# Kernel optimization log

Measured on AMD Instinct MI355X. Metric: run time of the kernel, lower is better.

## Reference

```python
import jax, jax.numpy as jnp
import numpy as np

N_NODES = 50000
N_EDGES = 640000
WIDTH = 128
K = 5
N_CONVS = 6  # 1 input + 4 hidden + 1 output ChebConv layers


def setup_inputs() -> dict:
    key = jax.random.key(0)
    k1, k2, k3, k4 = jax.random.split(key, 4)
    scale = 1.0 / np.sqrt(WIDTH)
    x = jax.random.normal(k1, (N_NODES, WIDTH), dtype=jnp.float32)
    edge_index = jax.random.randint(k2, (2, N_EDGES), 0, N_NODES, dtype=jnp.int64)
    conv_w = jax.random.normal(k3, (N_CONVS, K, WIDTH, WIDTH), dtype=jnp.float32) * scale
    conv_b = jnp.zeros((N_CONVS, WIDTH), dtype=jnp.float32)
    lin_w = jax.random.normal(k4, (WIDTH, 1), dtype=jnp.float32) * scale
    lin_b = jnp.zeros((1,), dtype=jnp.float32)
    return {"x": x, "edge_index": edge_index, "conv_w": conv_w,
            "conv_b": conv_b, "lin_w": lin_w, "lin_b": lin_b}


def _cheb_norm(edge_index):
    # PyG ChebConv with normalization='sym', lambda_max=2.0:
    # L_hat = 2/lambda_max * (I - D^-1/2 A D^-1/2) - I = -D^-1/2 A D^-1/2
    # (diagonal terms cancel), so per-edge weight = -d_i^-1/2 * d_j^-1/2.
    src, dst = edge_index[0], edge_index[1]
    ones = jnp.ones((edge_index.shape[1],), dtype=jnp.float32)
    deg = jax.ops.segment_sum(ones, dst, num_segments=N_NODES)
    d_inv_sqrt = jnp.where(deg > 0, jax.lax.rsqrt(jnp.maximum(deg, 1e-12)), 0.0)
    return -d_inv_sqrt[src] * d_inv_sqrt[dst]


def _propagate(x, src, dst, norm):
    # L_hat @ x via gather -> weight -> scatter-add
    msg = norm[:, None] * x[src]              # [E, C]
    return jax.ops.segment_sum(msg, dst, num_segments=N_NODES)


def _cheb_conv(x, W, b, src, dst, norm):
    # Chebyshev recurrence: T0=x, T1=Lx, Tk = 2*L*T(k-1) - T(k-2)
    Tx0 = x
    out = Tx0 @ W[0]
    Tx1 = _propagate(Tx0, src, dst, norm)
    out = out + Tx1 @ W[1]
    for k in range(2, K):
        Tx2 = 2.0 * _propagate(Tx1, src, dst, norm) - Tx0
        out = out + Tx2 @ W[k]
        Tx0, Tx1 = Tx1, Tx2
    return out + b


def reference(x, edge_index, conv_w, conv_b, lin_w, lin_b):
    src, dst = edge_index[0], edge_index[1]
    norm = _cheb_norm(edge_index)
    h = x
    # first 5 convs followed by ReLU (dropout is identity in eval mode)
    for l in range(N_CONVS - 1):
        h = _cheb_conv(h, conv_w[l], conv_b[l], src, dst, norm)
        h = jax.nn.relu(h)
    # final conv (no activation) + Linear(128, 1)
    h = _cheb_conv(h, conv_w[N_CONVS - 1], conv_b[N_CONVS - 1], src, dst, norm)
    return h @ lin_w + lin_b
```

## Files before the change

### kernel.cpp

```cpp
#include <hip/hip_runtime.h>


#define NN 50000
#define NE 640000
#define WID 128
#define PROP_BLOCKS 2048

typedef __attribute__((ext_vector_type(8))) short bf16x8;
typedef __attribute__((ext_vector_type(4))) float f32x4;

__device__ __forceinline__ unsigned short f2bf(float f) {
  union { float f; unsigned int u; } v; v.f = f;
  unsigned int r = v.u + 0x7FFF + ((v.u >> 16) & 1);
  return (unsigned short)(r >> 16);
}
__device__ __forceinline__ unsigned int pack2(float lo, float hi) {
  return (unsigned int)f2bf(lo) | ((unsigned int)f2bf(hi) << 16);
}
__device__ __forceinline__ float bflo(unsigned int u) {
  return __uint_as_float(u << 16);
}
__device__ __forceinline__ float bfhi(unsigned int u) {
  return __uint_as_float(u & 0xffff0000u);
}
__device__ __forceinline__ float dec_norm(unsigned int p) {
  unsigned int lo = p & 0xfffu;
  float v = -__uint_as_float(((112u + ((p >> 8) & 15u)) << 23) | ((p & 255u) << 15));
  return (lo == 0u) ? 0.f : v;
}


__global__ __launch_bounds__(256) void degree_kernel(const int* __restrict__ ei,
                                                     int* __restrict__ deg, int E) {
  int e = blockIdx.x * 256 + threadIdx.x;
  if (e < E) atomicAdd(&deg[ei[E + e]], 1);
}

__global__ __launch_bounds__(256) void scan1_kernel(const int* __restrict__ deg,
                                                    int* __restrict__ lex,
                                                    int* __restrict__ bsum,
                                                    float* __restrict__ dinv, int n) {
  __shared__ int ws[4];
  int tid = threadIdx.x, lane = tid & 63, w = tid >> 6;
  int i = blockIdx.x * 256 + tid;
  int cnt = (i < n) ? deg[i] : 0;
  if (i < n) {
    float d = (float)cnt;
    dinv[i] = d > 0.0f ? rsqrtf(d) : 0.0f;
  }
  int v = cnt;
#pragma unroll
  for (int off = 1; off < 64; off <<= 1) {
    int u = __shfl_up(v, off, 64);
    if (lane >= off) v += u;
  }
  if (lane == 63) ws[w] = v;
  __syncthreads();
  int wexcl = 0;
#pragma unroll
  for (int k = 0; k < 4; ++k) wexcl += (k < w) ? ws[k] : 0;
  if (i < n) lex[i] = wexcl + v - cnt;
  if (tid == 255) bsum[blockIdx.x] = wexcl + v;
}

__global__ __launch_bounds__(256) void scan2_kernel(const int* __restrict__ bsum,
                                                    int* __restrict__ boff,
                                                    int* __restrict__ row_end, int nb) {
  __shared__ int ws[4];
  int tid = threadIdx.x, lane = tid & 63, w = tid >> 6;
  int cnt = (tid < nb) ? bsum[tid] : 0;
  int v = cnt;
#pragma unroll
  for (int off = 1; off < 64; off <<= 1) {
    int u = __shfl_up(v, off, 64);
    if (lane >= off) v += u;
  }
  if (lane == 63) ws[w] = v;
  __syncthreads();
  int wexcl = 0;
#pragma unroll
  for (int k = 0; k < 4; ++k) wexcl += (k < w) ? ws[k] : 0;
  if (tid < nb) boff[tid] = wexcl + v - cnt;
  if (tid == 255) *row_end = wexcl + v;
}

__global__ __launch_bounds__(256) void scan3_kernel(const int* __restrict__ lex,
                                                    const int* __restrict__ boff,
                                                    int* __restrict__ row_start,
                                                    int* __restrict__ fill_ptr, int n) {
  int i = blockIdx.x * 256 + threadIdx.x;
  if (i < n) {
    int rs = lex[i] + boff[blockIdx.x];
    row_start[i] = rs;
    fill_ptr[i] = rs;
  }
}

__global__ __launch_bounds__(256) void fill_kernel(const int* __restrict__ ei,
                                                   const float* __restrict__ dinv,
                                                   int* __restrict__ fill_ptr,
                                                   unsigned int* __restrict__ csr, int E) {
  int e = blockIdx.x * 256 + threadIdx.x;
  if (e < E) {
    int s = ei[e];
    int d = ei[E + e];
    int pos = atomicAdd(&fill_ptr[d], 1);
    float mag = dinv[s] * dinv[d];
    unsigned int bits = __float_as_uint(mag);
    unsigned int pk = (unsigned int)s << 12;
    if (bits != 0u) {
      bits += 0x4000u;
      int ex = (int)((bits >> 23) & 255u) - 112;
      ex = max(0, min(15, ex));
      pk |= ((unsigned int)ex << 8) | ((bits >> 15) & 0xffu);
    }
    csr[pos] = pk;
  }
}

__global__ __launch_bounds__(256) void cvt_kernel(const float* __restrict__ x,
                                                  unsigned short* __restrict__ xo,
                                                  const float* __restrict__ w,
                                                  unsigned short* __restrict__ wt,
                                                  int nx, int nw) {
  int i = blockIdx.x * 256 + threadIdx.x;
  if (i < nx) {
    xo[i] = f2bf(x[i]);
  } else if (i < nx + nw) {
    int j = i - nx;
    int l = j / (WID * 640);
    int r = j % (WID * 640);
    int col = r / 640;
    int k = r % 640;
    int kk = k >> 7, m = k & 127;
    wt[j] = f2bf(w[(((size_t)l * 5 + kk) * WID + m) * WID + col]);
  }
}


__global__ __launch_bounds__(256) void prop_kernel(unsigned short* __restrict__ out,
                                                   const unsigned short* __restrict__ xin,
                                                   const unsigned short* __restrict__ sub,
                                                   float scale,
                                                   const int* __restrict__ row_start,
                                                   const unsigned int* __restrict__ csr,
                                                   int n) {
  int t = threadIdx.x & 15;
  for (int node = blockIdx.x * 16 + (threadIdx.x >> 4); node < n;
       node += PROP_BLOCKS * 16) {
    int s = row_start[node], e = row_start[node + 1];
    float a0 = 0.f, a1 = 0.f, a2 = 0.f, a3 = 0.f;
    float a4 = 0.f, a5 = 0.f, a6 = 0.f, a7 = 0.f;
    for (int base = s; base < e; base += 16) {
      int cnt = min(16, e - base);
      unsigned int ed = (t < cnt) ? csr[base + t] : 0u;
      int j = 0;
      for (; j + 4 <= cnt; j += 4) {
        unsigned int p0 = (unsigned int)__shfl((int)ed, j, 16);
        unsigned int p1 = (unsigned int)__shfl((int)ed, j + 1, 16);
        unsigned int p2 = (unsigned int)__shfl((int)ed, j + 2, 16);
        unsigned int p3 = (unsigned int)__shfl((int)ed, j + 3, 16);
        int s0 = p0 >> 12, s1 = p1 >> 12, s2 = p2 >> 12, s3 = p3 >> 12;
        float n0 = dec_norm(p0), n1 = dec_norm(p1), n2 = dec_norm(p2), n3 = dec_norm(p3);
        const uint4 v0 = *(const uint4*)(xin + (size_t)s0 * WID + t * 8);
        const uint4 v1 = *(const uint4*)(xin + (size_t)s1 * WID + t * 8);
        const uint4 v2 = *(const uint4*)(xin + (size_t)s2 * WID + t * 8);
        const uint4 v3 = *(const uint4*)(xin + (size_t)s3 * WID + t * 8);
        a0 += n0 * bflo(v0.x) + n1 * bflo(v1.x) + n2 * bflo(v2.x) + n3 * bflo(v3.x);
        a1 += n0 * bfhi(v0.x) + n1 * bfhi(v1.x) + n2 * bfhi(v2.x) + n3 * bfhi(v3.x);
        a2 += n0 * bflo(v0.y) + n1 * bflo(v1.y) + n2 * bflo(v2.y) + n3 * bflo(v3.y);
        a3 += n0 * bfhi(v0.y) + n1 * bfhi(v1.y) + n2 * bfhi(v2.y) + n3 * bfhi(v3.y);
        a4 += n0 * bflo(v0.z) + n1 * bflo(v1.z) + n2 * bflo(v2.z) + n3 * bflo(v3.z);
        a5 += n0 * bfhi(v0.z) + n1 * bfhi(v1.z) + n2 * bfhi(v2.z) + n3 * bfhi(v3.z);
        a6 += n0 * bflo(v0.w) + n1 * bflo(v1.w) + n2 * bflo(v2.w) + n3 * bflo(v3.w);
        a7 += n0 * bfhi(v0.w) + n1 * bfhi(v1.w) + n2 * bfhi(v2.w) + n3 * bfhi(v3.w);
      }
      for (; j < cnt; ++j) {
        unsigned int pj = (unsigned int)__shfl((int)ed, j, 16);
        int sj = pj >> 12;
        float nj = dec_norm(pj);
        const uint4 v = *(const uint4*)(xin + (size_t)sj * WID + t * 8);
        a0 += nj * bflo(v.x); a1 += nj * bfhi(v.x);
        a2 += nj * bflo(v.y); a3 += nj * bfhi(v.y);
        a4 += nj * bflo(v.z); a5 += nj * bfhi(v.z);
        a6 += nj * bflo(v.w); a7 += nj * bfhi(v.w);
      }
    }
    size_t o = (size_t)node * WID + t * 8;
    float r0 = scale * a0, r1 = scale * a1, r2 = scale * a2, r3 = scale * a3;
    float r4 = scale * a4, r5 = scale * a5, r6 = scale * a6, r7 = scale * a7;
    if (sub) {
      const uint4 sv = *(const uint4*)(sub + o);
      r0 -= bflo(sv.x); r1 -= bfhi(sv.x);
      r2 -= bflo(sv.y); r3 -= bfhi(sv.y);
      r4 -= bflo(sv.z); r5 -= bfhi(sv.z);
      r6 -= bflo(sv.w); r7 -= bfhi(sv.w);
    }
    uint4 wv;
    wv.x = pack2(r0, r1); wv.y = pack2(r2, r3);
    wv.z = pack2(r4, r5); wv.w = pack2(r6, r7);
    *(uint4*)(out + o) = wv;
  }
}


__global__ __launch_bounds__(256) void cheb_gemm(
    const unsigned short* __restrict__ T0, const unsigned short* __restrict__ T1,
    const unsigned short* __restrict__ T2, const unsigned short* __restrict__ T3,
    const unsigned short* __restrict__ T4,
    const unsigned short* __restrict__ Wt,
    const float* __restrict__ bias,
    unsigned short* __restrict__ Hb,
    const float* __restrict__ linw, const float* __restrict__ linb,
    float* __restrict__ y, int M, int mode) {
  __shared__ unsigned short As[64][72];
  __shared__ unsigned short Bs[128][72];
  const unsigned short* chunks[5] = {T0, T1, T2, T3, T4};
  int tid = threadIdx.x;
  int wave = tid >> 6, lane = tid & 63;
  int lrow = lane & 15, quad = lane >> 4;
  int rowBase = blockIdx.x * 64;

  f32x4 acc[8];
#pragma unroll
  for (int b = 0; b < 8; ++b) acc[b] = (f32x4){0.f, 0.f, 0.f, 0.f};

  int ar = tid >> 2, aseg = (tid & 3) * 16;
  int agrow = min(rowBase + ar, M - 1);
  int bc = tid >> 1, bseg = (tid & 1) * 32;

  int4 aR0, aR1, bR0, bR1, bR2, bR3;
  {
    const unsigned short* ap = chunks[0] + (size_t)agrow * WID + aseg;
    aR0 = *(const int4*)ap;
    aR1 = *(const int4*)(ap + 8);
    const unsigned short* bp = Wt + (size_t)bc * 640 + bseg;
    bR0 = *(const int4*)bp;
    bR1 = *(const int4*)(bp + 8);
    bR2 = *(const int4*)(bp + 16);
    bR3 = *(const int4*)(bp + 24);
  }

  for (int kc = 0; kc < 10; ++kc) {
    *(int4*)(&As[ar][aseg]) = aR0;
    *(int4*)(&As[ar][aseg + 8]) = aR1;
    *(int4*)(&Bs[bc][bseg]) = bR0;
    *(int4*)(&Bs[bc][bseg + 8]) = bR1;
    *(int4*)(&Bs[bc][bseg + 16]) = bR2;
    *(int4*)(&Bs[bc][bseg + 24]) = bR3;
    __syncthreads();

    if (kc < 9) {
      int kn = kc + 1;
      const unsigned short* ap =
          chunks[kn >> 1] + (size_t)agrow * WID + (kn & 1) * 64 + aseg;
      aR0 = *(const int4*)ap;
      aR1 = *(const int4*)(ap + 8);
      const unsigned short* bp = Wt + (size_t)bc * 640 + kn * 64 + bseg;
      bR0 = *(const int4*)bp;
      bR1 = *(const int4*)(bp + 8);
      bR2 = *(const int4*)(bp + 16);
      bR3 = *(const int4*)(bp + 24);
    }

    bf16x8 a0 = *(bf16x8*)(&As[wave * 16 + lrow][quad * 8]);
    bf16x8 a1 = *(bf16x8*)(&As[wave * 16 + lrow][32 + quad * 8]);
#pragma unroll
    for (int ct = 0; ct < 8; ++ct) {
      bf16x8 b0 = *(bf16x8*)(&Bs[ct * 16 + lrow][quad * 8]);
      acc[ct] = __builtin_amdgcn_mfma_f32_16x16x32_bf16(a0, b0, acc[ct], 0, 0, 0);
      bf16x8 b1 = *(bf16x8*)(&Bs[ct * 16 + lrow][32 + quad * 8]);
      acc[ct] = __builtin_amdgcn_mfma_f32_16x16x32_bf16(a1, b1, acc[ct], 0, 0, 0);
    }
    __syncthreads();
  }

  if (mode != 2) {
#pragma unroll
    for (int ct = 0; ct < 8; ++ct) {
      int gcol = ct * 16 + lrow;
      float bv = bias[gcol];
#pragma unroll
      for (int reg = 0; reg < 4; ++reg) {
        int grow = rowBase + wave * 16 + quad * 4 + reg;
        if (grow < M) {
          float v = acc[ct][reg] + bv;
          if (mode == 1) v = fmaxf(v, 0.f);
          Hb[(size_t)grow * WID + gcol] = f2bf(v);
        }
      }
    }
  } else {
    float lwv[8], bvv[8];
#pragma unroll
    for (int ct = 0; ct < 8; ++ct) {
      int gcol = ct * 16 + lrow;
      lwv[ct] = linw[gcol];
      bvv[ct] = bias[gcol];
    }
#pragma unroll
    for (int reg = 0; reg < 4; ++reg) {
      float part = 0.f;
#pragma unroll
      for (int ct = 0; ct < 8; ++ct) part += (acc[ct][reg] + bvv[ct]) * lwv[ct];
#pragma unroll
      for (int off = 1; off < 16; off <<= 1) part += __shfl_xor(part, off, 16);
      int grow = rowBase + wave * 16 + quad * 4 + reg;
      if (lrow == 0 && grow < M) y[grow] = part + linb[0];
    }
  }
}


extern "C" void kernel_launch(void* const* d_in, const int* in_sizes, int n_in,
                              void* d_out, int out_size, void* d_ws, size_t ws_size,
                              hipStream_t stream) {
  const float* x = (const float*)d_in[0];
  const int* ei = (const int*)d_in[1];
  const float* conv_w = (const float*)d_in[2];
  const float* conv_b = (const float*)d_in[3];
  const float* lin_w = (const float*)d_in[4];
  const float* lin_b = (const float*)d_in[5];

  const int N = NN, E = NE, C = WID, L = 6;
  const int NB = (N + 255) / 256;

  char* ws = (char*)d_ws;
  size_t off = 0;
  auto alloc = [&](size_t bytes) -> void* {
    void* p = ws + off;
    off = (off + bytes + 255) & ~(size_t)255;
    return p;
  };
  int* deg = (int*)alloc((size_t)N * 4);
  float* dinv = (float*)alloc((size_t)N * 4);
  int* row_start = (int*)alloc((size_t)(N + 1) * 4);
  int* fill_ptr = (int*)alloc((size_t)N * 4);
  int* lex = (int*)alloc((size_t)N * 4);
  int* bsum = (int*)alloc((size_t)NB * 4);
  int* boff = (int*)alloc((size_t)NB * 4);
  unsigned int* csr = (unsigned int*)alloc((size_t)E * 4);
  unsigned short* Xbf = (unsigned short*)alloc((size_t)N * C * 2);
  unsigned short* Hb0 = (unsigned short*)alloc((size_t)N * C * 2);
  unsigned short* Hb1 = (unsigned short*)alloc((size_t)N * C * 2);
  unsigned short* T1b = (unsigned short*)alloc((size_t)N * C * 2);
  unsigned short* T2b = (unsigned short*)alloc((size_t)N * C * 2);
  unsigned short* T3b = (unsigned short*)alloc((size_t)N * C * 2);
  unsigned short* T4b = (unsigned short*)alloc((size_t)N * C * 2);
  unsigned short* Wt = (unsigned short*)alloc((size_t)L * C * 640 * 2);

  hipMemsetAsync(deg, 0, (size_t)N * 4, stream);
  degree_kernel<<<(E + 255) / 256, 256, 0, stream>>>(ei, deg, E);
  scan1_kernel<<<NB, 256, 0, stream>>>(deg, lex, bsum, dinv, N);
  scan2_kernel<<<1, 256, 0, stream>>>(bsum, boff, &row_start[N], NB);
  scan3_kernel<<<NB, 256, 0, stream>>>(lex, boff, row_start, fill_ptr, N);
  fill_kernel<<<(E + 255) / 256, 256, 0, stream>>>(ei, dinv, fill_ptr, csr, E);
  {
    int nx = N * C, nw = L * C * 640;
    cvt_kernel<<<(nx + nw + 255) / 256, 256, 0, stream>>>(x, Xbf, conv_w, Wt, nx, nw);
  }

  const int gg = (N + 63) / 64;

  for (int l = 0; l < L; ++l) {
    const unsigned short* T0 = (l == 0) ? Xbf : ((l & 1) ? Hb0 : Hb1);
    unsigned short* Hb = (l & 1) ? Hb1 : Hb0;
    int mode = (l < L - 1) ? 1 : 2;

    prop_kernel<<<PROP_BLOCKS, 256, 0, stream>>>(T1b, T0, nullptr, 1.0f, row_start, csr, N);
    prop_kernel<<<PROP_BLOCKS, 256, 0, stream>>>(T2b, T1b, T0, 2.0f, row_start, csr, N);
    prop_kernel<<<PROP_BLOCKS, 256, 0, stream>>>(T3b, T2b, T1b, 2.0f, row_start, csr, N);
    prop_kernel<<<PROP_BLOCKS, 256, 0, stream>>>(T4b, T3b, T2b, 2.0f, row_start, csr, N);
    cheb_gemm<<<gg, 256, 0, stream>>>(T0, T1b, T2b, T3b, T4b,
                                      Wt + (size_t)l * C * 640, conv_b + (size_t)l * C,
                                      Hb, lin_w, lin_b, (float*)d_out, N, mode);
  }
}
```

Baseline: 908.4 us.

## Fold final linear projection into last ChebConv and propagate projected low-width features

The last ChebConv is followed by Linear(128,1), so the weights are precombined into per-order vectors V_k = W_k·lin_w. The final hidden state is then projected to 5 scalars per node, and the Chebyshev recurrence runs on these narrow vectors instead of 128-wide features. This removes four full-width propagations and one GEMM for the final layer. In exchange it adds small setup and projection kernels and changes the summation order, along with where bf16 rounding happens.

```diff
diff --git a/kernel.cpp b/kernel.cpp
--- a/kernel.cpp
+++ b/kernel.cpp
@@ -134,6 +134,28 @@
     int k = r % 640;
     int kk = k >> 7, m = k & 127;
     wt[j] = f2bf(w[(((size_t)l * 5 + kk) * WID + m) * WID + col]);
+  }
+}
+
+__global__ __launch_bounds__(256) void vk_kernel(const float* __restrict__ w,
+                                                 const float* __restrict__ b,
+                                                 const float* __restrict__ lw,
+                                                 const float* __restrict__ lb,
+                                                 float* __restrict__ V,
+                                                 float* __restrict__ cst) {
+  int tid = threadIdx.x;
+  for (int idx = tid; idx < 5 * WID; idx += 256) {
+    int k = idx / WID, i = idx % WID;
+    const float* wr = w + (((size_t)5 * 5 + k) * WID + i) * WID;
+    float s = 0.f;
+#pragma unroll 4
+    for (int j = 0; j < WID; ++j) s += wr[j] * lw[j];
+    V[idx] = s;
+  }
+  if (tid == 0) {
+    float s = 0.f;
+    for (int c = 0; c < WID; ++c) s += b[5 * WID + c] * lw[c];
+    *cst = s + lb[0];
   }
 }
 
@@ -203,6 +225,78 @@
   }
 }
 
+__global__ __launch_bounds__(256) void final_proj(const unsigned short* __restrict__ H,
+                                                  const float* __restrict__ V,
+                                                  const float* __restrict__ cstp,
+                                                  float* __restrict__ U,
+                                                  float* __restrict__ y, int n) {
+  int t = threadIdx.x & 15;
+  int node = blockIdx.x * 16 + (threadIdx.x >> 4);
+  if (node >= n) return;
+  const uint4 h = *(const uint4*)(H + (size_t)node * WID + t * 8);
+  float hv0 = bflo(h.x), hv1 = bfhi(h.x), hv2 = bflo(h.y), hv3 = bfhi(h.y);
+  float hv4 = bflo(h.z), hv5 = bfhi(h.z), hv6 = bflo(h.w), hv7 = bfhi(h.w);
+  float p[5];
+#pragma unroll
+  for (int k = 0; k < 5; ++k) {
+    const float4* vp = (const float4*)(V + k * WID + t * 8);
+    float4 v0 = vp[0], v1 = vp[1];
+    float s = hv0 * v0.x + hv1 * v0.y + hv2 * v0.z + hv3 * v0.w +
+              hv4 * v1.x + hv5 * v1.y + hv6 * v1.z + hv7 * v1.w;
+#pragma unroll
+    for (int off = 1; off < 16; off <<= 1) s += __shfl_xor(s, off, 16);
+    p[k] = s;
+  }
+  if (t == 0) {
+    float4 u0 = {p[0], p[1], p[2], p[3]};
+    float4 u1 = {p[4], 0.f, 0.f, 0.f};
+    *(float4*)(U + (size_t)node * 8) = u0;
+    *(float4*)(U + (size_t)node * 8 + 4) = u1;
+    y[node] = p[0] + *cstp;
+  }
+}
+
+__global__ __launch_bounds__(256) void prop_small(float* __restrict__ out,
+                                                  const float* __restrict__ xin,
+                                                  const float* __restrict__ sub,
+                                                  float scale, int pick,
+                                                  float* __restrict__ y,
+                                                  const int* __restrict__ row_start,
+                                                  const unsigned int* __restrict__ csr,
+                                                  int n) {
+  int node = blockIdx.x * 256 + threadIdx.x;
+  if (node >= n) return;
+  int s = row_start[node], e = row_start[node + 1];
+  float a0 = 0.f, a1 = 0.f, a2 = 0.f, a3 = 0.f;
+  float a4 = 0.f, a5 = 0.f, a6 = 0.f, a7 = 0.f;
+  for (int i = s; i < e; ++i) {
+    unsigned int p = csr[i];
+    int src = (int)(p >> 12);
+    float nv = dec_norm(p);
+    const float4* r = (const float4*)(xin + (size_t)src * 8);
+    float4 v0 = r[0], v1 = r[1];
+    a0 += nv * v0.x; a1 += nv * v0.y; a2 += nv * v0.z; a3 += nv * v0.w;
+    a4 += nv * v1.x; a5 += nv * v1.y; a6 += nv * v1.z; a7 += nv * v1.w;
+  }
+  float o0 = scale * a0, o1 = scale * a1, o2 = scale * a2, o3 = scale * a3;
+  float o4 = scale * a4, o5 = scale * a5, o6 = scale * a6, o7 = scale * a7;
+  if (sub) {
+    const float4* sv = (const float4*)(sub + (size_t)node * 8);
+    float4 s0 = sv[0], s1 = sv[1];
+    o0 -= s0.x; o1 -= s0.y; o2 -= s0.z; o3 -= s0.w;
+    o4 -= s1.x; o5 -= s1.y; o6 -= s1.z; o7 -= s1.w;
+  }
+  float4 w0 = {o0, o1, o2, o3};
+  float4 w1 = {o4, o5, o6, o7};
+  *(float4*)(out + (size_t)node * 8) = w0;
+  *(float4*)(out + (size_t)node * 8 + 4) = w1;
+  float yp = o1;
+  if (pick == 2) yp = o2;
+  if (pick == 3) yp = o3;
+  if (pick == 4) yp = o4;
+  y[node] += yp;
+}
+
 
 __global__ __launch_bounds__(256) void cheb_gemm(
     const unsigned short* __restrict__ T0, const unsigned short* __restrict__ T1,
@@ -210,9 +304,7 @@
     const unsigned short* __restrict__ T4,
     const unsigned short* __restrict__ Wt,
     const float* __restrict__ bias,
-    unsigned short* __restrict__ Hb,
-    const float* __restrict__ linw, const float* __restrict__ linb,
-    float* __restrict__ y, int M, int mode) {
+    unsigned short* __restrict__ Hb, int M) {
   __shared__ unsigned short As[64][72];
   __shared__ unsigned short Bs[128][72];
   const unsigned short* chunks[5] = {T0, T1, T2, T3, T4};
@@ -275,38 +367,17 @@
     __syncthreads();
   }
 
-  if (mode != 2) {
-#pragma unroll
-    for (int ct = 0; ct < 8; ++ct) {
-      int gcol = ct * 16 + lrow;
-      float bv = bias[gcol];
-#pragma unroll
-      for (int reg = 0; reg < 4; ++reg) {
-        int grow = rowBase + wave * 16 + quad * 4 + reg;
-        if (grow < M) {
-          float v = acc[ct][reg] + bv;
-          if (mode == 1) v = fmaxf(v, 0.f);
-          Hb[(size_t)grow * WID + gcol] = f2bf(v);
-        }
+#pragma unroll
+  for (int ct = 0; ct < 8; ++ct) {
+    int gcol = ct * 16 + lrow;
+    float bv = bias[gcol];
+#pragma unroll
+    for (int reg = 0; reg < 4; ++reg) {
+      int grow = rowBase + wave * 16 + quad * 4 + reg;
+      if (grow < M) {
+        float v = fmaxf(acc[ct][reg] + bv, 0.f);
+        Hb[(size_t)grow * WID + gcol] = f2bf(v);
       }
-    }
-  } else {
-    float lwv[8], bvv[8];
-#pragma unroll
-    for (int ct = 0; ct < 8; ++ct) {
-      int gcol = ct * 16 + lrow;
-      lwv[ct] = linw[gcol];
-      bvv[ct] = bias[gcol];
-    }
-#pragma unroll
-    for (int reg = 0; reg < 4; ++reg) {
-      float part = 0.f;
-#pragma unroll
-      for (int ct = 0; ct < 8; ++ct) part += (acc[ct][reg] + bvv[ct]) * lwv[ct];
-#pragma unroll
-      for (int off = 1; off < 16; off <<= 1) part += __shfl_xor(part, off, 16);
-      int grow = rowBase + wave * 16 + quad * 4 + reg;
-      if (lrow == 0 && grow < M) y[grow] = part + linb[0];
     }
   }
 }
@@ -347,7 +418,9 @@
   unsigned short* T2b = (unsigned short*)alloc((size_t)N * C * 2);
   unsigned short* T3b = (unsigned short*)alloc((size_t)N * C * 2);
   unsigned short* T4b = (unsigned short*)alloc((size_t)N * C * 2);
-  unsigned short* Wt = (unsigned short*)alloc((size_t)L * C * 640 * 2);
+  unsigned short* Wt = (unsigned short*)alloc((size_t)5 * C * 640 * 2);
+  float* V = (float*)alloc((size_t)5 * C * 4);
+  float* cst = (float*)alloc(4);
 
   hipMemsetAsync(deg, 0, (size_t)N * 4, stream);
   degree_kernel<<<(E + 255) / 256, 256, 0, stream>>>(ei, deg, E);
@@ -356,16 +429,16 @@
   scan3_kernel<<<NB, 256, 0, stream>>>(lex, boff, row_start, fill_ptr, N);
   fill_kernel<<<(E + 255) / 256, 256, 0, stream>>>(ei, dinv, fill_ptr, csr, E);
   {
-    int nx = N * C, nw = L * C * 640;
+    int nx = N * C, nw = 5 * C * 640;
     cvt_kernel<<<(nx + nw + 255) / 256, 256, 0, stream>>>(x, Xbf, conv_w, Wt, nx, nw);
   }
+  vk_kernel<<<1, 256, 0, stream>>>(conv_w, conv_b, lin_w, lin_b, V, cst);
 
   const int gg = (N + 63) / 64;
 
-  for (int l = 0; l < L; ++l) {
+  for (int l = 0; l < 5; ++l) {
     const unsigned short* T0 = (l == 0) ? Xbf : ((l & 1) ? Hb0 : Hb1);
     unsigned short* Hb = (l & 1) ? Hb1 : Hb0;
-    int mode = (l < L - 1) ? 1 : 2;
 
     prop_kernel<<<PROP_BLOCKS, 256, 0, stream>>>(T1b, T0, nullptr, 1.0f, row_start, csr, N);
     prop_kernel<<<PROP_BLOCKS, 256, 0, stream>>>(T2b, T1b, T0, 2.0f, row_start, csr, N);
@@ -373,6 +446,21 @@
     prop_kernel<<<PROP_BLOCKS, 256, 0, stream>>>(T4b, T3b, T2b, 2.0f, row_start, csr, N);
     cheb_gemm<<<gg, 256, 0, stream>>>(T0, T1b, T2b, T3b, T4b,
                                       Wt + (size_t)l * C * 640, conv_b + (size_t)l * C,
-                                      Hb, lin_w, lin_b, (float*)d_out, N, mode);
-  }
-}
+                                      Hb, N);
+  }
+
+  {
+    float* y = (float*)d_out;
+    float* U  = (float*)T1b;
+    float* P1 = (float*)T2b;
+    float* P2 = (float*)T3b;
+    float* P3 = (float*)T4b;
+    float* P4 = (float*)Xbf;
+    const int pg = (N + 255) / 256;
+    final_proj<<<(N + 15) / 16, 256, 0, stream>>>(Hb0, V, cst, U, y, N);
+    prop_small<<<pg, 256, 0, stream>>>(P1, U, nullptr, 1.0f, 1, y, row_start, csr, N);
+    prop_small<<<pg, 256, 0, stream>>>(P2, P1, U, 2.0f, 2, y, row_start, csr, N);
+    prop_small<<<pg, 256, 0, stream>>>(P3, P2, P1, 2.0f, 3, y, row_start, csr, N);
+    prop_small<<<pg, 256, 0, stream>>>(P4, P3, P2, 2.0f, 4, y, row_start, csr, N);
+  }
+}
```

New measurement: 859.0 us. -5.4%, faster.
